# Kernel optimization log

Measured on AMD Instinct MI355X. Metric: run time of the kernel, lower is better.

The kernel has to match this reference:

```python
import jax, jax.numpy as jnp
import numpy as np

B, S, D = 2, 2048, 1024
R = 64
H = 16
DH = D // H
N = 32  # neurons per bank (fqk, fv, rqk, rv)


def setup_inputs() -> dict:
    key = jax.random.key(0)
    ks = jax.random.split(key, 13)
    inp = {
        'x': jax.random.normal(ks[0], (B, S, D), dtype=jnp.float32),
        'fqk_weights_Q': jax.random.uniform(ks[1], (B, S, N), dtype=jnp.float32),
        'fqk_weights_K': jax.random.uniform(ks[2], (B, S, N), dtype=jnp.float32),
        'fv_weights': jax.random.uniform(ks[3], (B, S, N), dtype=jnp.float32),
        'rqk_weights_Q': jax.random.uniform(ks[4], (B, S, N), dtype=jnp.float32),
        'rqk_weights_K': jax.random.uniform(ks[5], (B, S, N), dtype=jnp.float32),
        'rv_weights': jax.random.uniform(ks[6], (B, S, N), dtype=jnp.float32),
        # neuron banks (orthogonal init in original; random normal is fine for numerics)
        'f_qk': jax.random.normal(ks[7], (N, D, R), dtype=jnp.float32) / np.sqrt(D),
        'f_v': jax.random.normal(ks[8], (N, D, R), dtype=jnp.float32) / np.sqrt(D),
        'r_qk': jax.random.normal(ks[9], (N, R, D), dtype=jnp.float32) / np.sqrt(R),
        'r_v': jax.random.normal(ks[10], (N, R, D), dtype=jnp.float32) / np.sqrt(R),
        'W_O': jax.random.normal(ks[11], (D, D), dtype=jnp.float32) / np.sqrt(D),  # torch Linear weight [out,in]
    }
    return inp


def _mix_project(x, w, neurons):
    # h[b,s,r] = sum_n w[b,s,n] * (x[b,s,:] @ neurons[n])  -- reassociated, avoids [B,S,D,R]
    p = jnp.einsum('bsd,ndr->bsnr', x, neurons)  # [B,S,N,R]
    return jnp.einsum('bsn,bsnr->bsr', w, p)


def _mix_restore(h, w, neurons):
    # y[b,s,d] = sum_n w[b,s,n] * (h[b,s,:] @ neurons[n])  -- reassociated, avoids [B,S,R,D]
    hw = jnp.einsum('bsr,bsn->bsnr', h, w)  # [B,S,N,R]
    return jnp.einsum('bsnr,nrd->bsd', hw, neurons)


def _causal_sdpa(Q, K, V):
    # Q,K,V: [B,H,S,DH]
    scale = 1.0 / np.sqrt(Q.shape[-1]).astype(np.float32)
    scores = jnp.einsum('bhqd,bhkd->bhqk', Q, K) * scale
    s = Q.shape[2]
    mask = jnp.tril(jnp.ones((s, s), dtype=bool))
    scores = jnp.where(mask, scores, jnp.finfo(scores.dtype).min)
    attn = jax.nn.softmax(scores, axis=-1)
    return jnp.einsum('bhqk,bhkd->bhqd', attn, V)


def reference(x, fqk_weights_Q, fqk_weights_K, fv_weights,
              rqk_weights_Q, rqk_weights_K, rv_weights,
              f_qk, f_v, r_qk, r_v, W_O):
    b, s, d = x.shape
    h_q = _mix_project(x, fqk_weights_Q, f_qk)  # [B,S,R]
    h_k = _mix_project(x, fqk_weights_K, f_qk)
    h_v = _mix_project(x, fv_weights, f_v)

    Q = _mix_restore(h_q, rqk_weights_Q, r_qk)  # [B,S,D]
    K = _mix_restore(h_k, rqk_weights_K, r_qk)
    V = _mix_restore(h_v, rv_weights, r_v)

    Q = Q.reshape(b, s, H, DH).transpose(0, 2, 1, 3)
    K = K.reshape(b, s, H, DH).transpose(0, 2, 1, 3)
    V = V.reshape(b, s, H, DH).transpose(0, 2, 1, 3)

    attn_out = _causal_sdpa(Q, K, V)  # [B,H,S,DH]
    attn_out = attn_out.transpose(0, 2, 1, 3).reshape(b, s, d)
    out = attn_out @ W_O.T  # nn.Linear(d, d, bias=False)
    return out
```

## Files before the change

### kernel.cpp

```cpp
#include <hip/hip_runtime.h>
#include <hip/hip_bf16.h>
#include <cstdint>
#include <cstddef>

typedef unsigned short u16;
typedef short bfrag __attribute__((ext_vector_type(8)));
typedef _Float16 hfrag __attribute__((ext_vector_type(8)));
typedef float f32x4 __attribute__((ext_vector_type(4)));
typedef u16 u16x8 __attribute__((ext_vector_type(8)));

__device__ __forceinline__ u16 f2bf(float v) {
    union { float f; unsigned u; } a; a.f = v;
    unsigned r = a.u + 0x7fff + ((a.u >> 16) & 1);
    return (u16)(r >> 16);
}
__device__ __forceinline__ float bf2f(u16 u) {
    union { unsigned u; float f; } a; a.u = ((unsigned)u) << 16;
    return a.f;
}
__device__ __forceinline__ u16 f2h(float v) {
    union { _Float16 h; u16 u; } a; a.h = (_Float16)v;
    return a.u;
}
__device__ __forceinline__ f32x4 mfma_bf16(bfrag a, bfrag b, f32x4 c) {
    return __builtin_amdgcn_mfma_f32_16x16x32_bf16(a, b, c, 0, 0, 0);
}
__device__ __forceinline__ f32x4 mfma_f16(hfrag a, hfrag b, f32x4 c) {
    return __builtin_amdgcn_mfma_f32_16x16x32_f16(a, b, c, 0, 0, 0);
}
__device__ __forceinline__ void async_copy16(const void* g, void* l) {
    __builtin_amdgcn_global_load_lds(
        (const __attribute__((address_space(1))) unsigned*)g,
        (__attribute__((address_space(3))) unsigned*)l, 16, 0, 0);
}
__device__ __forceinline__ int get_xcd() {
    unsigned x;
    asm volatile("s_getreg_b32 %0, hwreg(HW_REG_XCC_ID)" : "=s"(x));
    return (int)(x & 7);
}

template<int SPLIT>
__global__ __launch_bounds__(256) void cast_split(const float* __restrict__ s,
                                                  u16* __restrict__ dh,
                                                  u16* __restrict__ dl, int n4)
{
    int i = blockIdx.x * 256 + threadIdx.x;
    if (i >= n4) return;
    float4 v = ((const float4*)s)[i];
    float vv[4] = {v.x, v.y, v.z, v.w};
    ushort4 h, l;
    u16* hp = (u16*)&h; u16* lp = (u16*)&l;
#pragma unroll
    for (int e = 0; e < 4; ++e) {
        u16 hb = f2bf(vv[e]);
        hp[e] = hb;
        if (SPLIT) lp[e] = f2bf(vv[e] - bf2f(hb));
    }
    ((ushort4*)dh)[i] = h;
    if (SPLIT) ((ushort4*)dl)[i] = l;
}

template<int MODE>
__global__ __launch_bounds__(256) void transpose_cast(const float* __restrict__ src,
                                                      u16* __restrict__ dh,
                                                      u16* __restrict__ dl,
                                                      int R, int C, int dpitch)
{
    __shared__ float t[32][33];
    int z = blockIdx.z;
    const float* s = src + (size_t)z * R * C;
    int r0 = blockIdx.y * 32, c0 = blockIdx.x * 32;
    int tx = threadIdx.x & 31, ty = threadIdx.x >> 5;
#pragma unroll
    for (int p = 0; p < 4; ++p)
        t[ty + p * 8][tx] = s[(size_t)(r0 + ty + p * 8) * C + c0 + tx];
    __syncthreads();
#pragma unroll
    for (int p = 0; p < 4; ++p) {
        int rr = ty + p * 8;
        float v = t[tx][rr];
        size_t di = (size_t)(z * C + c0 + rr) * dpitch + r0 + tx;
        if (MODE == 2) {
            dh[di] = f2h(v);
        } else {
            u16 hb = f2bf(v);
            dh[di] = hb;
            if (MODE == 1) dl[di] = f2bf(v - bf2f(hb));
        }
    }
}

template<int SPLIT, int CTH>
__global__ __launch_bounds__(256) void gemm_mfma(const u16* __restrict__ Agh,
                                                 const u16* __restrict__ Agl,
                                                 const u16* __restrict__ Bgh,
                                                 const u16* __restrict__ Bgl,
                                                 float* __restrict__ C,
                                                 int M, int N, int K)
{
    constexpr int HB = SPLIT ? 16384 : 8192;
    __shared__ u16 lds[2 * HB];

    const int bid = blockIdx.x;
    const int xq  = bid & 7;
    const int s   = bid >> 3;
    const int RP  = (M >> 7) >> 3;
    const int rowt = xq * RP + (s % RP);
    const int ct   = s / RP;
    const int row0 = rowt * 128;
    const int col0 = ct * 128;

    const int tid  = threadIdx.x;
    const int lane = tid & 63;
    const int wv   = tid >> 6;
    const int q    = lane >> 4;
    const int tn   = lane & 15;
    const int wm   = (wv >> 1) * 64;
    const int wn   = (wv & 1) * 64;
    const int wbase = (tid & 192) * 8;

    auto stage = [&](u16* base, int k0) {
        u16* Ath = base;
        u16* Atl = SPLIT ? (base + 4096) : base;
        u16* Bth = base + (SPLIT ? 8192 : 4096);
        u16* Btl = SPLIT ? (base + 12288) : base;
#pragma unroll
        for (int shot = 0; shot < 2; ++shot) {
            int G = tid + shot * 256;
            int row = G >> 2, kgs = G & 3;
            int kgg = kgs ^ ((row >> 1) & 3);
            size_t goffB = (size_t)(col0 + row) * K + k0 + kgg * 8;
            async_copy16(Bgh + goffB, Bth + shot * 2048 + wbase);
            if (SPLIT) async_copy16(Bgl + goffB, Btl + shot * 2048 + wbase);
            size_t goffA = (size_t)(row0 + row) * K + k0 + kgg * 8;
            async_copy16(Agh + goffA, Ath + shot * 2048 + wbase);
            if (SPLIT) async_copy16(Agl + goffA, Atl + shot * 2048 + wbase);
        }
    };

    f32x4 acc[4][4];
#pragma unroll
    for (int i = 0; i < 4; ++i)
#pragma unroll
        for (int j = 0; j < 4; ++j) acc[i][j] = 0.f;

    stage(lds, 0);
    __syncthreads();

    int cur = 0;
    const int NT = K >> 5;
    for (int n = 0; n < NT; ++n) {
        if (n + 1 < NT) stage(lds + (cur ^ 1) * HB, (n + 1) * 32);

        const u16* base = lds + cur * HB;
        const u16* Ath = base;
        const u16* Atl = SPLIT ? (base + 4096) : base;
        const u16* Bth = base + (SPLIT ? 8192 : 4096);
        const u16* Btl = SPLIT ? (base + 12288) : base;

        bfrag ah[4], bh[4], al[4], bl[4];
#pragma unroll
        for (int i = 0; i < 4; ++i) {
            int m = wm + i * 16 + tn;
            int g = m * 4 + (q ^ ((m >> 1) & 3));
            ah[i] = *(const bfrag*)(Ath + g * 8);
            if (SPLIT) al[i] = *(const bfrag*)(Atl + g * 8);
        }
#pragma unroll
        for (int j = 0; j < 4; ++j) {
            int n2 = wn + j * 16 + tn;
            int g = n2 * 4 + (q ^ ((n2 >> 1) & 3));
            bh[j] = *(const bfrag*)(Bth + g * 8);
            if (SPLIT) bl[j] = *(const bfrag*)(Btl + g * 8);
        }
#pragma unroll
        for (int i = 0; i < 4; ++i)
#pragma unroll
            for (int j = 0; j < 4; ++j) {
                acc[i][j] = mfma_bf16(ah[i], bh[j], acc[i][j]);
                if (SPLIT) {
                    acc[i][j] = mfma_bf16(ah[i], bl[j], acc[i][j]);
                    acc[i][j] = mfma_bf16(al[i], bh[j], acc[i][j]);
                }
            }
        __syncthreads();
        cur ^= 1;
    }

#pragma unroll
    for (int i = 0; i < 4; ++i)
#pragma unroll
        for (int j = 0; j < 4; ++j)
#pragma unroll
            for (int rg = 0; rg < 4; ++rg) {
                int row = row0 + wm + i * 16 + q * 4 + rg;
                int col = col0 + wn + j * 16 + tn;
                C[(size_t)row * N + col] = acc[i][j][rg];
            }
}

__global__ __launch_bounds__(256) void build_ahw(
    const float* __restrict__ h_q, const float* __restrict__ wQ,
    const float* __restrict__ h_k, const float* __restrict__ wK,
    const float* __restrict__ h_v, const float* __restrict__ wV,
    u16* __restrict__ Ahw)
{
    const int b   = blockIdx.x;
    const int sel = b >> 12;
    const int row = b & 4095;
    const float* h = (sel == 0) ? h_q : (sel == 1) ? h_k : h_v;
    const float* w = (sel == 0) ? wQ  : (sel == 1) ? wK  : wV;
    const int kg = threadIdx.x;
    const float wm = w[(size_t)row * 32 + (kg >> 3)];
    const float* hp = h + (size_t)row * 64 + (kg & 7) * 8;
    float4 v0 = *(const float4*)hp;
    float4 v1 = *(const float4*)(hp + 4);
    float vv[8] = {v0.x, v0.y, v0.z, v0.w, v1.x, v1.y, v1.z, v1.w};
    u16x8 o;
#pragma unroll
    for (int e = 0; e < 8; ++e) o[e] = f2h(vv[e] * wm);
    *(u16x8*)(Ahw + (((size_t)sel * 4096 + row) * 2048) + kg * 8) = o;
}

__global__ __launch_bounds__(256) void restore_mega(
    const u16* __restrict__ Ahw,
    const u16* __restrict__ Rqk, const u16* __restrict__ Rv,
    u16* __restrict__ Qf, u16* __restrict__ Kf, u16* __restrict__ Vt,
    int* __restrict__ queue)
{
    __shared__ int sjob;
    __shared__ u16 lds[8192];
    u16* Ath = lds;
    u16* Bth = lds + 4096;

    const int tid = threadIdx.x;
    if (tid == 0) {
        int xcd = get_xcd();
        int job = -1;
        for (int t = 0; t < 8; ++t) {
            int qi = (xcd + t) & 7;
            int j = atomicAdd(&queue[qi], 1);
            if (j < 96) { job = qi * 96 + j; break; }
        }
        sjob = job;
    }
    __syncthreads();
    const int job = sjob;
    if (job < 0) return;
    const int qi   = job / 96;
    const int j    = job % 96;
    const int p    = qi * 12 + (j >> 3);
    const int sel  = p >> 5;
    const int rowt = p & 31;
    const int ct   = j & 7;
    const u16* Ag = Ahw + (size_t)sel * 4096 * 2048;
    const u16* Bg = (sel < 2) ? Rqk : Rv;
    const int K = 2048;
    const int row0 = rowt * 128, col0 = ct * 128;

    const int lane = tid & 63;
    const int wv   = tid >> 6;
    const int q    = lane >> 4;
    const int tn   = lane & 15;
    const int wm   = (wv >> 1) * 64;
    const int wn   = (wv & 1) * 64;
    const int wbase = (tid & 192) * 8;

    f32x4 acc[4][4];
#pragma unroll
    for (int i = 0; i < 4; ++i)
#pragma unroll
        for (int jj2 = 0; jj2 < 4; ++jj2) acc[i][jj2] = 0.f;

    for (int k0 = 0; k0 < K; k0 += 32) {
#pragma unroll
        for (int shot = 0; shot < 2; ++shot) {
            int G = tid + shot * 256;
            int row = G >> 2, kgs = G & 3;
            int kgg = kgs ^ ((row >> 1) & 3);
            size_t goffB = (size_t)(col0 + row) * K + k0 + kgg * 8;
            async_copy16(Bg + goffB, Bth + shot * 2048 + wbase);
            size_t goffA = (size_t)(row0 + row) * K + k0 + kgg * 8;
            async_copy16(Ag + goffA, Ath + shot * 2048 + wbase);
        }
        __syncthreads();

        hfrag ah[4], bh[4];
#pragma unroll
        for (int i = 0; i < 4; ++i) {
            int m = wm + i * 16 + tn;
            int g = m * 4 + (q ^ ((m >> 1) & 3));
            ah[i] = *(const hfrag*)(Ath + g * 8);
        }
#pragma unroll
        for (int jj2 = 0; jj2 < 4; ++jj2) {
            int n = wn + jj2 * 16 + tn;
            int g = n * 4 + (q ^ ((n >> 1) & 3));
            bh[jj2] = *(const hfrag*)(Bth + g * 8);
        }
#pragma unroll
        for (int i = 0; i < 4; ++i)
#pragma unroll
            for (int jj2 = 0; jj2 < 4; ++jj2)
                acc[i][jj2] = mfma_f16(ah[i], bh[jj2], acc[i][jj2]);
        __syncthreads();
    }

#pragma unroll
    for (int i = 0; i < 4; ++i)
#pragma unroll
        for (int jj2 = 0; jj2 < 4; ++jj2)
#pragma unroll
            for (int rg = 0; rg < 4; ++rg) {
                int row = row0 + wm + i * 16 + q * 4 + rg;
                int col = col0 + wn + jj2 * 16 + tn;
                float v = acc[i][jj2][rg];
                if (sel < 2) {
                    size_t ix = (((size_t)(row >> 11) * 16 + (col >> 6)) << 17)
                              | ((size_t)(row & 2047) << 6) | (size_t)(col & 63);
                    ((sel == 0) ? Qf : Kf)[ix] = f2h(v);
                } else {
                    size_t ix = ((((size_t)(row >> 11) * 16 + (col >> 6)) * 64
                                 + (size_t)(col & 63)) << 11) | (size_t)(row & 2047);
                    Vt[ix] = f2h(v);
                }
            }
}

__global__ __launch_bounds__(256) void mix_kernel(const float* __restrict__ P,
                                                  const float* __restrict__ w1,
                                                  const float* __restrict__ w2,
                                                  float* __restrict__ h1,
                                                  float* __restrict__ h2,
                                                  int two)
{
    int tid = blockIdx.x * 256 + threadIdx.x;
    int bs = tid >> 6;
    int r  = tid & 63;
    const float* Pp = P + (size_t)bs * 2048 + r;
    float a = 0.f, b = 0.f;
#pragma unroll
    for (int n = 0; n < 32; ++n) {
        float p = Pp[n * 64];
        a = fmaf(w1[bs * 32 + n], p, a);
        if (two) b = fmaf(w2[bs * 32 + n], p, b);
    }
    h1[tid] = a;
    if (two) h2[tid] = b;
}

template<int SHOTS>
__device__ __forceinline__ void stage_tile(u16* dst, const u16* src, int rowstride,
                                           int tid, int wuni)
{
#pragma unroll
    for (int shot = 0; shot < SHOTS; ++shot) {
        int sl = shot * 256 + tid;
        int m = sl >> 3, s = sl & 7, g = s ^ (m & 7);
        async_copy16(src + (size_t)m * rowstride + g * 8, dst + shot * 2048 + wuni);
    }
}

__global__ __launch_bounds__(256) void flash_part(const u16* __restrict__ Qf_g,
                                                  const u16* __restrict__ Kf_g,
                                                  const u16* __restrict__ Vt_g,
                                                  u16* __restrict__ Opart,
                                                  float* __restrict__ ml)
{
    const int bid = blockIdx.x;
    const int idx = bid >> 3;
    const int bh  = (bid & 7) + 8 * (idx & 3);
    const int rest = idx >> 2;
    const int qb = 31 - (rest >> 3);
    const int c  = rest & 7;
    const int g  = qb >> 2, rr = qb & 3;
    const int nch = g + 1;
    if (c >= nch) return;
    const int q0 = qb * 64;
    const int slot = bh * 144 + (qb + 2 * g * (g - 1) + rr * g) + c;

    const int tid = threadIdx.x;
    const int lane = tid & 63;
    const int wv = tid >> 6;
    const int q = lane >> 4;
    const int tn = lane & 15;
    const int wuni = (tid & 192) * 8;

    __shared__ u16 sQ[4096], sK[4096], sV[4096], sP[4096];

    const size_t qoff = ((size_t)bh * 2048 + q0) * 64;
    stage_tile<2>(sQ, Qf_g + qoff, 64, tid, wuni);
    __syncthreads();

    hfrag qf[2];
#pragma unroll
    for (int ks = 0; ks < 2; ++ks) {
        int m = wv * 16 + tn;
        int slt = (ks * 4 + q) ^ (m & 7);
        qf[ks] = *(const hfrag*)(sQ + m * 64 + slt * 8);
    }

    float m_i[4], l_i[4];
    f32x4 acc_o[4];
#pragma unroll
    for (int ri = 0; ri < 4; ++ri) { m_i[ri] = -3.0e38f; l_i[ri] = 0.f; }
#pragma unroll
    for (int dt = 0; dt < 4; ++dt) acc_o[dt] = 0.f;

    const size_t kbase = (size_t)bh * 2048 * 64;
    const size_t vbase = (size_t)bh * 64 * 2048;
    const int kt_end = min(4 * c + 3, qb);

    for (int kt = 4 * c; kt <= kt_end; ++kt) {
        const int k0 = kt * 64;
        __syncthreads();
        stage_tile<2>(sK, Kf_g + kbase + (size_t)k0 * 64, 64, tid, wuni);
        stage_tile<2>(sV, Vt_g + vbase + k0, 2048, tid, wuni);
        __syncthreads();

        f32x4 accs[4];
#pragma unroll
        for (int n = 0; n < 4; ++n) accs[n] = 0.f;
#pragma unroll
        for (int n = 0; n < 4; ++n) {
            int r = n * 16 + tn;
#pragma unroll
            for (int ks = 0; ks < 2; ++ks) {
                int slt = (ks * 4 + q) ^ (r & 7);
                hfrag kf = *(const hfrag*)(sK + r * 64 + slt * 8);
                accs[n] = mfma_f16(qf[ks], kf, accs[n]);
            }
        }
        const bool diag = (kt == qb);
#pragma unroll
        for (int n = 0; n < 4; ++n)
#pragma unroll
            for (int ri = 0; ri < 4; ++ri) {
                float v = accs[n][ri] * 0.125f;
                if (diag && (n * 16 + tn > wv * 16 + q * 4 + ri)) v = -3.0e38f;
                accs[n][ri] = v;
            }
        float alpha[4], mnew[4], ssum[4];
#pragma unroll
        for (int ri = 0; ri < 4; ++ri) {
            float mx = fmaxf(fmaxf(accs[0][ri], accs[1][ri]),
                             fmaxf(accs[2][ri], accs[3][ri]));
#pragma unroll
            for (int xm = 1; xm < 16; xm <<= 1)
                mx = fmaxf(mx, __shfl_xor(mx, xm, 64));
            mnew[ri] = fmaxf(m_i[ri], mx);
            alpha[ri] = __expf(m_i[ri] - mnew[ri]);
            m_i[ri] = mnew[ri];
            ssum[ri] = 0.f;
        }
#pragma unroll
        for (int n = 0; n < 4; ++n)
#pragma unroll
            for (int ri = 0; ri < 4; ++ri) {
                float p = __expf(accs[n][ri] - mnew[ri]);
                ssum[ri] += p;
                int m = wv * 16 + q * 4 + ri;
                int cc = n * 16 + tn;
                int slt = (cc >> 3) ^ (m & 7);
                sP[m * 64 + slt * 8 + (cc & 7)] = f2h(p);
            }
#pragma unroll
        for (int ri = 0; ri < 4; ++ri) {
            float sm = ssum[ri];
#pragma unroll
            for (int xm = 1; xm < 16; xm <<= 1)
                sm += __shfl_xor(sm, xm, 64);
            l_i[ri] = l_i[ri] * alpha[ri] + sm;
#pragma unroll
            for (int dt = 0; dt < 4; ++dt) acc_o[dt][ri] *= alpha[ri];
        }
#pragma unroll
        for (int ks = 0; ks < 2; ++ks) {
            int m = wv * 16 + tn;
            int slt = (ks * 4 + q) ^ (m & 7);
            hfrag pf = *(const hfrag*)(sP + m * 64 + slt * 8);
#pragma unroll
            for (int dt = 0; dt < 4; ++dt) {
                int d = dt * 16 + tn;
                int vslt = (ks * 4 + q) ^ (d & 7);
                hfrag vf = *(const hfrag*)(sV + d * 64 + vslt * 8);
                acc_o[dt] = mfma_f16(pf, vf, acc_o[dt]);
            }
        }
    }

#pragma unroll
    for (int dt = 0; dt < 4; ++dt)
#pragma unroll
        for (int ri = 0; ri < 4; ++ri) {
            int row = wv * 16 + q * 4 + ri;
            Opart[(size_t)slot * 4096 + row * 64 + dt * 16 + tn] = f2bf(acc_o[dt][ri]);
        }
    if (tn == 0) {
#pragma unroll
        for (int ri = 0; ri < 4; ++ri) {
            int row = wv * 16 + q * 4 + ri;
            ml[(size_t)slot * 128 + row]      = m_i[ri];
            ml[(size_t)slot * 128 + 64 + row] = l_i[ri];
        }
    }
}

__global__ __launch_bounds__(256) void flash_combine(const u16* __restrict__ Opart,
                                                     const float* __restrict__ ml,
                                                     u16* __restrict__ Am)
{
    const int qb = blockIdx.x, bh = blockIdx.y;
    const int g = qb >> 2, rr = qb & 3;
    const int nch = g + 1;
    const int base = bh * 144 + (qb + 2 * g * (g - 1) + rr * g);
    const int tid = threadIdx.x;
    const int row = tid >> 2;
    const int c0  = (tid & 3) * 16;

    float mstar = -3.0e38f;
    float mc[8];
#pragma unroll
    for (int c = 0; c < 8; ++c) {
        if (c < nch) {
            mc[c] = ml[(size_t)(base + c) * 128 + row];
            mstar = fmaxf(mstar, mc[c]);
        }
    }
    float lstar = 0.f, wc[8];
#pragma unroll
    for (int c = 0; c < 8; ++c) {
        if (c < nch) {
            wc[c] = __expf(mc[c] - mstar);
            lstar += ml[(size_t)(base + c) * 128 + 64 + row] * wc[c];
        }
    }
    float o[16];
#pragma unroll
    for (int j = 0; j < 16; ++j) o[j] = 0.f;
    for (int c = 0; c < nch; ++c) {
        const u16* p = Opart + (size_t)(base + c) * 4096 + row * 64 + c0;
        u16x8 v0 = *(const u16x8*)p;
        u16x8 v1 = *(const u16x8*)(p + 8);
#pragma unroll
        for (int j = 0; j < 8; ++j) {
            o[j]     = fmaf(bf2f(v0[j]), wc[c], o[j]);
            o[j + 8] = fmaf(bf2f(v1[j]), wc[c], o[j + 8]);
        }
    }
    float inv = 1.0f / lstar;
    int srow = qb * 64 + row;
    size_t obase = ((size_t)(bh >> 4) * 2048 + srow) * 1024
                 + (size_t)((bh & 15) * 64 + c0);
    u16x8 w0, w1;
#pragma unroll
    for (int j = 0; j < 8; ++j) {
        w0[j] = f2bf(o[j] * inv);
        w1[j] = f2bf(o[j + 8] * inv);
    }
    *(u16x8*)(Am + obase)     = w0;
    *(u16x8*)(Am + obase + 8) = w1;
}

extern "C" void kernel_launch(void* const* d_in, const int* in_sizes, int n_in,
                              void* d_out, int out_size, void* d_ws, size_t ws_size,
                              hipStream_t stream)
{
    const float* x     = (const float*)d_in[0];
    const float* wfqkQ = (const float*)d_in[1];
    const float* wfqkK = (const float*)d_in[2];
    const float* wfv   = (const float*)d_in[3];
    const float* wrqkQ = (const float*)d_in[4];
    const float* wrqkK = (const float*)d_in[5];
    const float* wrv   = (const float*)d_in[6];
    const float* f_qk  = (const float*)d_in[7];
    const float* f_v   = (const float*)d_in[8];
    const float* r_qk  = (const float*)d_in[9];
    const float* r_v   = (const float*)d_in[10];
    const float* W_O   = (const float*)d_in[11];
    float* out = (float*)d_out;

    const size_t MB = 1u << 20;
    char* w8 = (char*)d_ws;
    u16*  WOb   = (u16*)(w8 + 0);
    u16*  x_hi  = (u16*)(w8 + 2  * MB);
    u16*  x_lo  = (u16*)(w8 + 10 * MB);
    u16*  FqkTh = (u16*)(w8 + 18 * MB);
    u16*  FqkTl = (u16*)(w8 + 22 * MB);
    u16*  FvT   = (u16*)(w8 + 26 * MB);
    u16*  RqkT  = (u16*)(w8 + 30 * MB);
    u16*  RvT   = (u16*)(w8 + 34 * MB);
    float* h_q  = (float*)(w8 + 38 * MB);
    float* h_k  = (float*)(w8 + 39 * MB);
    float* h_v  = (float*)(w8 + 40 * MB);
    int*  queue = (int*)(w8 + 41 * MB);
    u16*  Ahw   = (u16*)(w8 + 42 * MB);
    float* P    = (float*)(w8 + 48 * MB);
    u16*  Qf    = (u16*)(w8 + 2  * MB);
    u16*  Kf    = (u16*)(w8 + 10 * MB);
    u16*  Vt    = (u16*)(w8 + 18 * MB);
    u16*  Opart = (u16*)(w8 + 28 * MB);
    float* mlws = (float*)(w8 + 64 * MB);
    u16*  Am    = (u16*)(w8 + 67 * MB);

    dim3 blk(256);

    cast_split<1><<<dim3(4096), blk, 0, stream>>>(x, x_hi, x_lo, 1024 * 1024);
    cast_split<0><<<dim3(1024), blk, 0, stream>>>(W_O, WOb, nullptr, 256 * 1024);
    transpose_cast<1><<<dim3(2, 32, 32), blk, 0, stream>>>(f_qk, FqkTh, FqkTl, 1024, 64, 1024);
    transpose_cast<0><<<dim3(2, 32, 32), blk, 0, stream>>>(f_v,  FvT,   nullptr, 1024, 64, 1024);
    transpose_cast<2><<<dim3(32, 64, 1), blk, 0, stream>>>(r_qk, RqkT, nullptr, 2048, 1024, 2048);
    transpose_cast<2><<<dim3(32, 64, 1), blk, 0, stream>>>(r_v,  RvT,  nullptr, 2048, 1024, 2048);

    gemm_mfma<1, 2><<<dim3(512), blk, 0, stream>>>(x_hi, x_lo, FqkTh, FqkTl, P,
                                                   4096, 2048, 1024);
    mix_kernel<<<dim3(1024), blk, 0, stream>>>(P, wfqkQ, wfqkK, h_q, h_k, 1);
    gemm_mfma<0, 2><<<dim3(512), blk, 0, stream>>>(x_hi, nullptr, FvT, nullptr, P,
                                                   4096, 2048, 1024);
    mix_kernel<<<dim3(1024), blk, 0, stream>>>(P, wfv, nullptr, h_v, nullptr, 0);

    build_ahw<<<dim3(3 * 4096), blk, 0, stream>>>(h_q, wrqkQ, h_k, wrqkK, h_v, wrv, Ahw);
    hipMemsetAsync(queue, 0, 8 * sizeof(int), stream);
    restore_mega<<<dim3(768), blk, 0, stream>>>(Ahw, RqkT, RvT, Qf, Kf, Vt, queue);

    flash_part<<<dim3(8192), blk, 0, stream>>>(Qf, Kf, Vt, Opart, mlws);
    flash_combine<<<dim3(32, 32), blk, 0, stream>>>(Opart, mlws, Am);

    gemm_mfma<0, 1><<<dim3(256), blk, 0, stream>>>(Am, nullptr, WOb, nullptr, out,
                                                   4096, 1024, 1024);
}
```

Measured before the change: 411.5 us.

## Replace atomic job queue in restore GEMM with static XCD mapping and K=64 tiles

The restore GEMM drops its atomic per-XCD work queue, along with the memset that reset it, and derives each block's job directly from blockIdx, relying on round-robin dispatch to place blocks of the same queue on the same XCD. The K step per iteration doubles from 32 to 64, using a 64-wide swizzled LDS tile staged through the shared stage_tile helper. This halves the number of barrier pairs per tile and removes the atomic and memset overhead, at the cost of doubled LDS use, which may lower occupancy.

```diff
diff --git a/kernel.cpp b/kernel.cpp
--- a/kernel.cpp
+++ b/kernel.cpp
@@ -32,11 +32,6 @@
     __builtin_amdgcn_global_load_lds(
         (const __attribute__((address_space(1))) unsigned*)g,
         (__attribute__((address_space(3))) unsigned*)l, 16, 0, 0);
-}
-__device__ __forceinline__ int get_xcd() {
-    unsigned x;
-    asm volatile("s_getreg_b32 %0, hwreg(HW_REG_XCC_ID)" : "=s"(x));
-    return (int)(x & 7);
 }
 
 template<int SPLIT>
@@ -222,35 +217,32 @@
     *(u16x8*)(Ahw + (((size_t)sel * 4096 + row) * 2048) + kg * 8) = o;
 }
 
+template<int SHOTS>
+__device__ __forceinline__ void stage_tile(u16* dst, const u16* src, int rowstride,
+                                           int tid, int wuni)
+{
+#pragma unroll
+    for (int shot = 0; shot < SHOTS; ++shot) {
+        int sl = shot * 256 + tid;
+        int m = sl >> 3, s = sl & 7, g = s ^ (m & 7);
+        async_copy16(src + (size_t)m * rowstride + g * 8, dst + shot * 2048 + wuni);
+    }
+}
+
 __global__ __launch_bounds__(256) void restore_mega(
     const u16* __restrict__ Ahw,
     const u16* __restrict__ Rqk, const u16* __restrict__ Rv,
-    u16* __restrict__ Qf, u16* __restrict__ Kf, u16* __restrict__ Vt,
-    int* __restrict__ queue)
-{
-    __shared__ int sjob;
-    __shared__ u16 lds[8192];
+    u16* __restrict__ Qf, u16* __restrict__ Kf, u16* __restrict__ Vt)
+{
+    __shared__ u16 lds[16384];
     u16* Ath = lds;
-    u16* Bth = lds + 4096;
-
-    const int tid = threadIdx.x;
-    if (tid == 0) {
-        int xcd = get_xcd();
-        int job = -1;
-        for (int t = 0; t < 8; ++t) {
-            int qi = (xcd + t) & 7;
-            int j = atomicAdd(&queue[qi], 1);
-            if (j < 96) { job = qi * 96 + j; break; }
-        }
-        sjob = job;
-    }
-    __syncthreads();
-    const int job = sjob;
-    if (job < 0) return;
-    const int qi   = job / 96;
-    const int j    = job % 96;
-    const int p    = qi * 12 + (j >> 3);
-    const int sel  = p >> 5;
+    u16* Bth = lds + 8192;
+
+    const int bid = blockIdx.x;
+    const int qi  = bid & 7;
+    const int j   = bid >> 3;
+    const int p   = qi * 12 + (j >> 3);
+    const int sel = p >> 5;
     const int rowt = p & 31;
     const int ct   = j & 7;
     const u16* Ag = Ahw + (size_t)sel * 4096 * 2048;
@@ -258,63 +250,59 @@
     const int K = 2048;
     const int row0 = rowt * 128, col0 = ct * 128;
 
+    const int tid  = threadIdx.x;
     const int lane = tid & 63;
     const int wv   = tid >> 6;
     const int q    = lane >> 4;
     const int tn   = lane & 15;
     const int wm   = (wv >> 1) * 64;
     const int wn   = (wv & 1) * 64;
-    const int wbase = (tid & 192) * 8;
+    const int wuni = (tid & 192) * 8;
 
     f32x4 acc[4][4];
 #pragma unroll
     for (int i = 0; i < 4; ++i)
 #pragma unroll
-        for (int jj2 = 0; jj2 < 4; ++jj2) acc[i][jj2] = 0.f;
-
-    for (int k0 = 0; k0 < K; k0 += 32) {
-#pragma unroll
-        for (int shot = 0; shot < 2; ++shot) {
-            int G = tid + shot * 256;
-            int row = G >> 2, kgs = G & 3;
-            int kgg = kgs ^ ((row >> 1) & 3);
-            size_t goffB = (size_t)(col0 + row) * K + k0 + kgg * 8;
-            async_copy16(Bg + goffB, Bth + shot * 2048 + wbase);
-            size_t goffA = (size_t)(row0 + row) * K + k0 + kgg * 8;
-            async_copy16(Ag + goffA, Ath + shot * 2048 + wbase);
-        }
+        for (int jj = 0; jj < 4; ++jj) acc[i][jj] = 0.f;
+
+    for (int k0 = 0; k0 < K; k0 += 64) {
+        stage_tile<4>(Ath, Ag + (size_t)row0 * K + k0, K, tid, wuni);
+        stage_tile<4>(Bth, Bg + (size_t)col0 * K + k0, K, tid, wuni);
         __syncthreads();
 
-        hfrag ah[4], bh[4];
-#pragma unroll
-        for (int i = 0; i < 4; ++i) {
-            int m = wm + i * 16 + tn;
-            int g = m * 4 + (q ^ ((m >> 1) & 3));
-            ah[i] = *(const hfrag*)(Ath + g * 8);
-        }
-#pragma unroll
-        for (int jj2 = 0; jj2 < 4; ++jj2) {
-            int n = wn + jj2 * 16 + tn;
-            int g = n * 4 + (q ^ ((n >> 1) & 3));
-            bh[jj2] = *(const hfrag*)(Bth + g * 8);
-        }
-#pragma unroll
-        for (int i = 0; i < 4; ++i)
-#pragma unroll
-            for (int jj2 = 0; jj2 < 4; ++jj2)
-                acc[i][jj2] = mfma_f16(ah[i], bh[jj2], acc[i][jj2]);
+#pragma unroll
+        for (int sub = 0; sub < 2; ++sub) {
+            hfrag ah[4], bh[4];
+#pragma unroll
+            for (int i = 0; i < 4; ++i) {
+                int m = wm + i * 16 + tn;
+                int slt = (sub * 4 + q) ^ (m & 7);
+                ah[i] = *(const hfrag*)(Ath + m * 64 + slt * 8);
+            }
+#pragma unroll
+            for (int jj = 0; jj < 4; ++jj) {
+                int n = wn + jj * 16 + tn;
+                int slt = (sub * 4 + q) ^ (n & 7);
+                bh[jj] = *(const hfrag*)(Bth + n * 64 + slt * 8);
+            }
+#pragma unroll
+            for (int i = 0; i < 4; ++i)
+#pragma unroll
+                for (int jj = 0; jj < 4; ++jj)
+                    acc[i][jj] = mfma_f16(ah[i], bh[jj], acc[i][jj]);
+        }
         __syncthreads();
     }
 
 #pragma unroll
     for (int i = 0; i < 4; ++i)
 #pragma unroll
-        for (int jj2 = 0; jj2 < 4; ++jj2)
+        for (int jj = 0; jj < 4; ++jj)
 #pragma unroll
             for (int rg = 0; rg < 4; ++rg) {
                 int row = row0 + wm + i * 16 + q * 4 + rg;
-                int col = col0 + wn + jj2 * 16 + tn;
-                float v = acc[i][jj2][rg];
+                int col = col0 + wn + jj * 16 + tn;
+                float v = acc[i][jj][rg];
                 if (sel < 2) {
                     size_t ix = (((size_t)(row >> 11) * 16 + (col >> 6)) << 17)
                               | ((size_t)(row & 2047) << 6) | (size_t)(col & 63);
@@ -347,18 +335,6 @@
     }
     h1[tid] = a;
     if (two) h2[tid] = b;
-}
-
-template<int SHOTS>
-__device__ __forceinline__ void stage_tile(u16* dst, const u16* src, int rowstride,
-                                           int tid, int wuni)
-{
-#pragma unroll
-    for (int shot = 0; shot < SHOTS; ++shot) {
-        int sl = shot * 256 + tid;
-        int m = sl >> 3, s = sl & 7, g = s ^ (m & 7);
-        async_copy16(src + (size_t)m * rowstride + g * 8, dst + shot * 2048 + wuni);
-    }
 }
 
 __global__ __launch_bounds__(256) void flash_part(const u16* __restrict__ Qf_g,
@@ -593,7 +569,6 @@
     float* h_q  = (float*)(w8 + 38 * MB);
     float* h_k  = (float*)(w8 + 39 * MB);
     float* h_v  = (float*)(w8 + 40 * MB);
-    int*  queue = (int*)(w8 + 41 * MB);
     u16*  Ahw   = (u16*)(w8 + 42 * MB);
     float* P    = (float*)(w8 + 48 * MB);
     u16*  Qf    = (u16*)(w8 + 2  * MB);
@@ -620,8 +595,7 @@
     mix_kernel<<<dim3(1024), blk, 0, stream>>>(P, wfv, nullptr, h_v, nullptr, 0);
 
     build_ahw<<<dim3(3 * 4096), blk, 0, stream>>>(h_q, wrqkQ, h_k, wrqkK, h_v, wrv, Ahw);
-    hipMemsetAsync(queue, 0, 8 * sizeof(int), stream);
-    restore_mega<<<dim3(768), blk, 0, stream>>>(Ahw, RqkT, RvT, Qf, Kf, Vt, queue);
+    restore_mega<<<dim3(768), blk, 0, stream>>>(Ahw, RqkT, RvT, Qf, Kf, Vt);
 
     flash_part<<<dim3(8192), blk, 0, stream>>>(Qf, Kf, Vt, Opart, mlws);
     flash_combine<<<dim3(32, 32), blk, 0, stream>>>(Opart, mlws, Am);
```

New measurement: 413.1 us. Within noise of the previous version (+0.4%).
